# Kernel optimization log

Measured on AMD Instinct MI355X. Metric: run time of the kernel, lower is better.

The kernel has to match this reference:

```python
import jax, jax.numpy as jnp
import numpy as np

N_HEADS = 16


def setup_inputs() -> dict:
    key = jax.random.key(0)
    ks = jax.random.split(key, 9)
    B, S, D = 2, 2048, 1024
    s = 0.02
    return {
        "x": jax.random.normal(ks[0], (B, S, D), dtype=jnp.float32),
        "Wq": jax.random.normal(ks[1], (D, D), dtype=jnp.float32) * s,
        "bq": jax.random.normal(ks[2], (D,), dtype=jnp.float32) * s,
        "Wk": jax.random.normal(ks[3], (D, D), dtype=jnp.float32) * s,
        "bk": jax.random.normal(ks[4], (D,), dtype=jnp.float32) * s,
        "Wv": jax.random.normal(ks[5], (D, D), dtype=jnp.float32) * s,
        "bv": jax.random.normal(ks[6], (D,), dtype=jnp.float32) * s,
        "Wo": jax.random.normal(ks[7], (D, D), dtype=jnp.float32) * s,
        "bo": jax.random.normal(ks[8], (D,), dtype=jnp.float32) * s,
    }


def reference(x, Wq, bq, Wk, bk, Wv, bv, Wo, bo):
    B, S, D = x.shape
    H = N_HEADS
    hd = D // H
    # projections -> [B, H, S, hd]
    def heads(w, b):
        return (x @ w + b).reshape(B, S, H, hd).transpose(0, 2, 1, 3)
    Q, K, V = heads(Wq, bq), heads(Wk, bk), heads(Wv, bv)
    scores = jnp.einsum("bhqd,bhkd->bhqk", Q, K)
    causal = jnp.triu(jnp.ones((S, S), dtype=bool), k=1)  # True above diagonal
    scores = jnp.where(causal, -jnp.inf, scores)
    w = jax.nn.softmax(scores / jnp.sqrt(jnp.float32(hd)), axis=-1)
    ctx = jnp.einsum("bhqk,bhkd->bhqd", w, V).transpose(0, 2, 1, 3).reshape(B, S, D)
    return ctx @ Wo + bo
```

## Files before the change

kernel.cpp:

```cpp
#include <hip/hip_runtime.h>
#include <hip/hip_bf16.h>

typedef __attribute__((ext_vector_type(8))) short short8;
typedef __attribute__((ext_vector_type(4))) float floatx4;
typedef __attribute__((ext_vector_type(4))) int intx4;
typedef __attribute__((ext_vector_type(2))) int intx2;

#define D_MODEL 1024
#define SEQ     2048
#define NB      2
#define NH      16
#define HD      64
#define MROWS   4096
#define CZ      (0.125f * 1.44269504f)

__device__ __forceinline__ floatx4 mfma_bf16(short8 a, short8 b, floatx4 c) {
  return __builtin_amdgcn_mfma_f32_16x16x32_bf16(a, b, c, 0, 0, 0);
}

__device__ __forceinline__ void dma16(const __hip_bfloat16* g, __hip_bfloat16* l) {
  __builtin_amdgcn_global_load_lds(
      (const __attribute__((address_space(1))) void*)g,
      (__attribute__((address_space(3))) void*)l, 16, 0, 0);
}
#define WAIT_VM(n)  __asm__ __volatile__("s_waitcnt vmcnt(" #n ")" ::: "memory")
#define BARRIER()   __asm__ __volatile__("s_barrier" ::: "memory")
#define WAIT_LGKM() __asm__ __volatile__("s_waitcnt lgkmcnt(0)" ::: "memory")

__device__ __forceinline__ int pack2bf(float a, float b) {
  unsigned ua = __builtin_bit_cast(unsigned, a) + 0x8000u;
  unsigned ub = __builtin_bit_cast(unsigned, b) + 0x8000u;
  return (int)__builtin_amdgcn_perm(ub, ua, 0x07060302u);
}

__device__ __forceinline__ int cvtpk(float a, float b) {
  int r;
  __asm__("v_cvt_pk_bf16_f32 %0, %1, %2" : "=v"(r) : "v"(a), "v"(b));
  return r;
}

__global__ void prep_kernel(const float* __restrict__ x, __hip_bfloat16* __restrict__ xb,
                            const float* __restrict__ W0, const float* __restrict__ W1,
                            const float* __restrict__ W2, const float* __restrict__ W3,
                            __hip_bfloat16* __restrict__ T0, __hip_bfloat16* __restrict__ T1,
                            __hip_bfloat16* __restrict__ T2, __hip_bfloat16* __restrict__ T3) {
  const int z = blockIdx.z;
  if (z == 4) {
    const int tid = threadIdx.y * 32 + threadIdx.x;
    const int base = ((blockIdx.y * 32 + blockIdx.x) * 256 + tid) * 16;
#pragma unroll
    for (int c = 0; c < 4; c++) {
      float4 v = *(const float4*)(x + base + c * 4);
      __hip_bfloat16 tmp[4];
      tmp[0] = __float2bfloat16(v.x);
      tmp[1] = __float2bfloat16(v.y);
      tmp[2] = __float2bfloat16(v.z);
      tmp[3] = __float2bfloat16(v.w);
      *(ushort4*)(xb + base + c * 4) = *(ushort4*)tmp;
    }
    return;
  }
  const float* W = (z == 0) ? W0 : (z == 1) ? W1 : (z == 2) ? W2 : W3;
  __hip_bfloat16* Wt = (z == 0) ? T0 : (z == 1) ? T1 : (z == 2) ? T2 : T3;
  __shared__ float tile[32][33];
  int k0 = blockIdx.x * 32, n0 = blockIdx.y * 32;
  int tx = threadIdx.x, ty = threadIdx.y;
#pragma unroll
  for (int i = 0; i < 4; i++)
    tile[ty + 8 * i][tx] = W[(size_t)(k0 + ty + 8 * i) * D_MODEL + n0 + tx];
  __syncthreads();
#pragma unroll
  for (int i = 0; i < 4; i++)
    Wt[(size_t)(n0 + ty + 8 * i) * D_MODEL + k0 + tx] = __float2bfloat16(tile[tx][ty + 8 * i]);
}

template <int MODE>
__global__ __launch_bounds__(256) void gemm_kernel(
    const __hip_bfloat16* __restrict__ X,
    const __hip_bfloat16* __restrict__ Wt0, const __hip_bfloat16* __restrict__ Wt1,
    const __hip_bfloat16* __restrict__ Wt2,
    const float* __restrict__ b0, const float* __restrict__ b1, const float* __restrict__ b2,
    void* __restrict__ out0, void* __restrict__ out1, void* __restrict__ out2) {
  constexpr int MT = (MODE == 0) ? 128 : 64;
  constexpr int I = MT / 32;
  constexpr int NKT = D_MODEL / 32;
  constexpr int SMEM_BYTES = 3 * (MT * 32 + 128 * 32) * 2;

  const int z = blockIdx.y;
  const __hip_bfloat16* Wt = (z == 0) ? Wt0 : (z == 1) ? Wt1 : Wt2;
  const float* bias = (z == 0) ? b0 : (z == 1) ? b1 : b2;
  void* outp = (z == 0) ? out0 : (z == 1) ? out1 : out2;
  const float scale = (MODE == 0 && z == 0) ? CZ : 1.f;

  __shared__ __attribute__((aligned(16))) char smem[SMEM_BYTES];
  __hip_bfloat16* As = (__hip_bfloat16*)smem;
  __hip_bfloat16* Bs = (__hip_bfloat16*)smem + 3 * MT * 32;
  float* Es = (float*)smem;

  const int n0 = blockIdx.x * 128;
  const int m0 = blockIdx.z * MT;
  const int t = threadIdx.x;
  const int lane = t & 63, w = t >> 6;
  const int wm = (w >> 1) * (MT / 2), wn = (w & 1) * 64;
  const int lr = lane & 15;
  const int lq = lane >> 4;

  const __hip_bfloat16* Xp = X + (size_t)m0 * D_MODEL;
  const __hip_bfloat16* Wp = Wt + (size_t)n0 * D_MODEL;

  const int lrow = lane >> 2;
  const int skg = (lane & 3) << 3;
  const int srowA = ((MT == 128) ? (w << 5) : (w << 4)) + lrow;
  const int sbA0 = (((MT == 128) ? (w << 5) : (w << 4)) << 5);
  const int sbA1 = sbA0 + (16 << 5);
  const int srowB = (w << 5) + lrow;
  const int sbB0 = ((w << 5) << 5);
  const int sbB1 = sbB0 + (16 << 5);

#define STAGE_G(kt_, buf_)                                                              \
  {                                                                                     \
    const int kn_ = (kt_) * 32;                                                         \
    __hip_bfloat16* A_ = As + (buf_) * (MT * 32);                                       \
    __hip_bfloat16* B_ = Bs + (buf_) * (128 * 32);                                      \
    dma16(Xp + (size_t)srowA * D_MODEL + kn_ + skg, A_ + sbA0);                         \
    if (MT == 128) dma16(Xp + (size_t)(srowA + 16) * D_MODEL + kn_ + skg, A_ + sbA1);   \
    dma16(Wp + (size_t)srowB * D_MODEL + kn_ + skg, B_ + sbB0);                         \
    dma16(Wp + (size_t)(srowB + 16) * D_MODEL + kn_ + skg, B_ + sbB1);                  \
  }

  floatx4 acc[I][4];
#pragma unroll
  for (int i = 0; i < I; i++)
#pragma unroll
    for (int j = 0; j < 4; j++) acc[i][j] = (floatx4){0.f, 0.f, 0.f, 0.f};

  STAGE_G(0, 0);
  STAGE_G(1, 1);

  int cb = 0;
  for (int kt = 0; kt < NKT; kt++) {
    if (kt < NKT - 1) {
      if constexpr (MODE == 0) WAIT_VM(4);
      else                     WAIT_VM(3);
    } else {
      WAIT_VM(0);
    }
    BARRIER();
    if (kt + 2 < NKT) {
      const int nb = (cb == 0) ? 2 : cb - 1;
      STAGE_G(kt + 2, nb);
    }
    const __hip_bfloat16* Ac = As + cb * (MT * 32);
    const __hip_bfloat16* Bc = Bs + cb * (128 * 32);
    short8 af[I], bfr[4];
#pragma unroll
    for (int i = 0; i < I; i++) af[i] = *(const short8*)&Ac[(wm + i * 16 + lr) * 32 + lq * 8];
#pragma unroll
    for (int j = 0; j < 4; j++) bfr[j] = *(const short8*)&Bc[(wn + j * 16 + lr) * 32 + lq * 8];
#pragma unroll
    for (int i = 0; i < I; i++)
#pragma unroll
      for (int j = 0; j < 4; j++) acc[i][j] = mfma_bf16(af[i], bfr[j], acc[i][j]);
    cb = (cb == 2) ? 0 : cb + 1;
  }
#undef STAGE_G

  float bvj[4];
#pragma unroll
  for (int j = 0; j < 4; j++) bvj[j] = bias[n0 + wn + j * 16 + lr];

  if constexpr (MODE == 1) {
    BARRIER();
#pragma unroll
    for (int i = 0; i < I; i++) {
      const int rowb = wm + i * 16 + lq * 4;
#pragma unroll
      for (int j = 0; j < 4; j++)
#pragma unroll
        for (int r = 0; r < 4; r++)
          Es[(rowb + r) * 132 + wn + j * 16 + lr] = acc[i][j][r] + bvj[j];
    }
    WAIT_LGKM();
    BARRIER();
    const int L = t >> 2, nseg = (t & 3) * 32;
    float* op = (float*)outp + (size_t)(m0 + L) * D_MODEL + n0 + nseg;
    const float* src = &Es[L * 132 + nseg];
#pragma unroll
    for (int k = 0; k < 8; k++) *(float4*)(op + 4 * k) = *(const float4*)(src + 4 * k);
  } else if (z != 2) {
    for (int c = 0; c < 2; c++) {
      BARRIER();
#pragma unroll
      for (int i2 = 0; i2 < 2; i2++) {
        const int i = 2 * c + i2;
        const int rowb = (w >> 1) * 32 + i2 * 16 + lq * 4;
#pragma unroll
        for (int j = 0; j < 4; j++)
#pragma unroll
          for (int r = 0; r < 4; r++)
            Es[(rowb + r) * 132 + wn + j * 16 + lr] = (acc[i][j][r] + bvj[j]) * scale;
      }
      WAIT_LGKM();
      BARRIER();
      const int L = t >> 2, nseg = (t & 3) * 32;
      const int m = m0 + ((L >> 5) << 6) + (c << 5) + (L & 31);
      const int bb = m >> 11, s = m & 2047;
      const int nn = n0 + nseg;
      __hip_bfloat16* op = (__hip_bfloat16*)outp +
          (((size_t)(bb * NH + (nn >> 6)) * SEQ + s) * HD + (nn & 63));
      const float* src = &Es[L * 132 + nseg];
#pragma unroll
      for (int k = 0; k < 4; k++) {
        intx4 pk;
        pk[0] = pack2bf(src[8 * k + 0], src[8 * k + 1]);
        pk[1] = pack2bf(src[8 * k + 2], src[8 * k + 3]);
        pk[2] = pack2bf(src[8 * k + 4], src[8 * k + 5]);
        pk[3] = pack2bf(src[8 * k + 6], src[8 * k + 7]);
        *(intx4*)(op + 8 * k) = pk;
      }
    }
  } else {
    for (int c = 0; c < 2; c++) {
      BARRIER();
#pragma unroll
      for (int j2 = 0; j2 < 2; j2++) {
        const int j = 2 * c + j2;
        const int nl = ((w & 1) << 5) + (j2 << 4) + lr;
#pragma unroll
        for (int i = 0; i < I; i++) {
          const int moff = (w >> 1) * 64 + i * 16 + lq * 4;
          floatx4 v = acc[i][j];
          v[0] += bvj[j]; v[1] += bvj[j]; v[2] += bvj[j]; v[3] += bvj[j];
          *(floatx4*)&Es[nl * 132 + moff] = v;
        }
      }
      WAIT_LGKM();
      BARRIER();
      const int nl = t >> 2, mseg = (t & 3) * 32;
      const int n = n0 + ((nl >> 5) << 6) + (c << 5) + (nl & 31);
      const int s0 = m0 & 2047, bb = m0 >> 11;
      __hip_bfloat16* op = (__hip_bfloat16*)outp +
          (((size_t)(bb * NH + (n >> 6)) * HD + (n & 63)) * SEQ + s0 + mseg);
      const float* src = &Es[nl * 132 + mseg];
#pragma unroll
      for (int k = 0; k < 4; k++) {
        intx4 pk;
        pk[0] = pack2bf(src[8 * k + 0], src[8 * k + 1]);
        pk[1] = pack2bf(src[8 * k + 2], src[8 * k + 3]);
        pk[2] = pack2bf(src[8 * k + 4], src[8 * k + 5]);
        pk[3] = pack2bf(src[8 * k + 6], src[8 * k + 7]);
        *(intx4*)(op + 8 * k) = pk;
      }
    }
  }
}

__global__ __launch_bounds__(256, 4) void attn_kernel(
    const __hip_bfloat16* __restrict__ Q, const __hip_bfloat16* __restrict__ Kg,
    const __hip_bfloat16* __restrict__ Vt, __hip_bfloat16* __restrict__ ctx) {
  const int bh = blockIdx.x;
  const int b = bh >> 4, h = bh & 15;
  const int qt = 31 - blockIdx.y;
  const int t = threadIdx.x, lane = t & 63, w = t >> 6;
  const int lr = lane & 15, lq = lane >> 4;
  const int wr = w & 1, wb = w >> 1;

  __shared__ __attribute__((aligned(16))) __hip_bfloat16 Ks[2][64 * 64];
  __shared__ __attribute__((aligned(16))) __hip_bfloat16 VTs[2][64 * 64];

  const __hip_bfloat16* Qb = Q + (size_t)bh * SEQ * HD;
  const __hip_bfloat16* Kb = Kg + (size_t)bh * SEQ * HD;
  const __hip_bfloat16* Vb = Vt + (size_t)bh * HD * SEQ;

  const int qrow0 = qt * 64 + wr * 32;

  short8 qf[2][2];
#pragma unroll
  for (int rt = 0; rt < 2; rt++)
#pragma unroll
    for (int ks = 0; ks < 2; ks++)
      qf[rt][ks] = *(const short8*)(Qb + (size_t)(qrow0 + rt * 16 + lr) * HD + ks * 32 + lq * 8);

  const int srow = (w << 4) + (lane >> 3);
  const int sgl = lane & 7;
  const int sb0 = (w << 4) << 6;
  const int sb1 = ((w << 4) + 8) << 6;

#define STAGE(tb, nb)                                                                  \
  {                                                                                    \
    const int r0 = srow, r1 = srow + 8;                                                \
    dma16(Kb + ((size_t)((tb) + r0) << 6) + ((sgl ^ (r0 & 7)) << 3), &Ks[nb][sb0]);    \
    dma16(Kb + ((size_t)((tb) + r1) << 6) + ((sgl ^ (r1 & 7)) << 3), &Ks[nb][sb1]);    \
    dma16(Vb + (size_t)r0 * SEQ + (tb) + ((sgl ^ (r0 & 7)) << 3), &VTs[nb][sb0]);      \
    dma16(Vb + (size_t)r1 * SEQ + (tb) + ((sgl ^ (r1 & 7)) << 3), &VTs[nb][sb1]);      \
  }

  const int nkt = qt + 1;
  STAGE(0, 0);

  floatx4 o[2][4];
#pragma unroll
  for (int rt = 0; rt < 2; rt++)
#pragma unroll
    for (int dt = 0; dt < 4; dt++) o[rt][dt] = (floatx4){0.f, 0.f, 0.f, 0.f};
  floatx4 lsacc[2];
  lsacc[0] = (floatx4){0.f, 0.f, 0.f, 0.f};
  lsacc[1] = (floatx4){0.f, 0.f, 0.f, 0.f};

  short8 ones;
#pragma unroll
  for (int j = 0; j < 8; j++) ones[j] = (short)0x3F80;

  const int kfb0 = ((wb << 4) + lr) << 6;
  const int kg0 = ((lq ^ (lr & 7)) << 3);
  const int kg1 = (((4 + lq) ^ (lr & 7)) << 3);
  const int vga = (((wb * 2 + (lq >> 1)) ^ (lr & 7)) << 3) + ((lq & 1) << 2);
  const int vgb = (((4 + wb * 2 + (lq >> 1)) ^ (lr & 7)) << 3) + ((lq & 1) << 2);

  for (int kt = 0; kt < nkt; kt++) {
    WAIT_VM(0);
    BARRIER();
    if (kt + 1 < nkt) STAGE((kt + 1) << 6, (kt + 1) & 1);

    const int kw0 = (kt << 6) + (wb << 4);
    if (kw0 <= qrow0 + 31) {
      const __hip_bfloat16* Kc = Ks[kt & 1];
      const __hip_bfloat16* Vc = VTs[kt & 1];

      short8 kf[2][2];
#pragma unroll
      for (int nt = 0; nt < 2; nt++) {
        kf[0][nt] = *(const short8*)&Kc[(nt << 11) + kfb0 + kg0];
        kf[1][nt] = *(const short8*)&Kc[(nt << 11) + kfb0 + kg1];
      }
      floatx4 s[2][2];
#pragma unroll
      for (int rt = 0; rt < 2; rt++)
#pragma unroll
        for (int nt = 0; nt < 2; nt++) s[rt][nt] = (floatx4){0.f, 0.f, 0.f, 0.f};
#pragma unroll
      for (int ks = 0; ks < 2; ks++)
#pragma unroll
        for (int nt = 0; nt < 2; nt++) {
          s[0][nt] = mfma_bf16(kf[ks][nt], qf[0][ks], s[0][nt]);
          s[1][nt] = mfma_bf16(kf[ks][nt], qf[1][ks], s[1][nt]);
        }

      const bool need_mask = (kw0 + 47 > qrow0);
      short8 pf[2];
#pragma unroll
      for (int rt = 0; rt < 2; rt++) {
        const int q = qrow0 + rt * 16 + lr;
        intx4 pk;
#pragma unroll
        for (int nt = 0; nt < 2; nt++) {
          const int kbase = (kt << 6) + (nt << 5) + (wb << 4) + (lq << 2);
          float x0 = s[rt][nt][0], x1 = s[rt][nt][1], x2 = s[rt][nt][2], x3 = s[rt][nt][3];
          if (need_mask) {
            x0 = (kbase + 0 <= q) ? x0 : -1e30f;
            x1 = (kbase + 1 <= q) ? x1 : -1e30f;
            x2 = (kbase + 2 <= q) ? x2 : -1e30f;
            x3 = (kbase + 3 <= q) ? x3 : -1e30f;
          }
          const float p0 = __builtin_amdgcn_exp2f(x0);
          const float p1 = __builtin_amdgcn_exp2f(x1);
          const float p2 = __builtin_amdgcn_exp2f(x2);
          const float p3 = __builtin_amdgcn_exp2f(x3);
          pk[2 * nt + 0] = cvtpk(p0, p1);
          pk[2 * nt + 1] = cvtpk(p2, p3);
        }
        pf[rt] = __builtin_bit_cast(short8, pk);
      }

      lsacc[0] = mfma_bf16(ones, pf[0], lsacc[0]);
      lsacc[1] = mfma_bf16(ones, pf[1], lsacc[1]);

#pragma unroll
      for (int dt = 0; dt < 4; dt++) {
        const int rb = ((dt << 4) + lr) << 6;
        intx4 vi;
        *(intx2*)&vi = *(const intx2*)&Vc[rb + vga];
        *(((intx2*)&vi) + 1) = *(const intx2*)&Vc[rb + vgb];
        short8 vf = __builtin_bit_cast(short8, vi);
        o[0][dt] = mfma_bf16(vf, pf[0], o[0][dt]);
        o[1][dt] = mfma_bf16(vf, pf[1], o[1][dt]);
      }
    }
  }

  BARRIER();
  if (wb == 1) {
    float* d0 = (float*)&Ks[0][0];
    float* d1 = (float*)&Ks[1][0];
    float* dl = (float*)&VTs[0][0];
    const int base = (wr << 10) + (lane << 4);
#pragma unroll
    for (int dt = 0; dt < 4; dt++) *(floatx4*)&d0[base + (dt << 2)] = o[0][dt];
#pragma unroll
    for (int dt = 0; dt < 4; dt++) *(floatx4*)&d1[base + (dt << 2)] = o[1][dt];
    dl[(wr << 7) + (lane << 1)] = lsacc[0][0];
    dl[(wr << 7) + (lane << 1) + 1] = lsacc[1][0];
    WAIT_LGKM();
  }
  BARRIER();
  if (wb == 0) {
    const float* d0 = (const float*)&Ks[0][0];
    const float* d1 = (const float*)&Ks[1][0];
    const float* dl = (const float*)&VTs[0][0];
    const int base = (wr << 10) + (lane << 4);
#pragma unroll
    for (int dt = 0; dt < 4; dt++) {
      o[0][dt] += *(const floatx4*)&d0[base + (dt << 2)];
      o[1][dt] += *(const floatx4*)&d1[base + (dt << 2)];
    }
    float inv[2];
    inv[0] = 1.f / (lsacc[0][0] + dl[(wr << 7) + (lane << 1)]);
    inv[1] = 1.f / (lsacc[1][0] + dl[(wr << 7) + (lane << 1) + 1]);
#pragma unroll
    for (int rt = 0; rt < 2; rt++) {
      const int row = qrow0 + rt * 16 + lr;
      __hip_bfloat16* cp = ctx + (size_t)b * SEQ * D_MODEL + (size_t)row * D_MODEL + h * HD;
#pragma unroll
      for (int dt = 0; dt < 4; dt++) {
        ushort4 pk;
        __hip_bfloat16* pp = (__hip_bfloat16*)&pk;
#pragma unroll
        for (int r = 0; r < 4; r++) pp[r] = __float2bfloat16(o[rt][dt][r] * inv[rt]);
        *(ushort4*)(cp + (dt << 4) + (lq << 2)) = pk;
      }
    }
  }
#undef STAGE
}

extern "C" void kernel_launch(void* const* d_in, const int* in_sizes, int n_in,
                              void* d_out, int out_size, void* d_ws, size_t ws_size,
                              hipStream_t stream) {
  const float* x  = (const float*)d_in[0];
  const float* Wq = (const float*)d_in[1];
  const float* bq = (const float*)d_in[2];
  const float* Wk = (const float*)d_in[3];
  const float* bk = (const float*)d_in[4];
  const float* Wv = (const float*)d_in[5];
  const float* bv = (const float*)d_in[6];
  const float* Wo = (const float*)d_in[7];
  const float* bo = (const float*)d_in[8];

  char* ws = (char*)d_ws;
  const size_t MB = 1u << 20;
  __hip_bfloat16* xb  = (__hip_bfloat16*)(ws + 0 * MB);
  __hip_bfloat16* wtq = (__hip_bfloat16*)(ws + 8 * MB);
  __hip_bfloat16* wtk = (__hip_bfloat16*)(ws + 10 * MB);
  __hip_bfloat16* wtv = (__hip_bfloat16*)(ws + 12 * MB);
  __hip_bfloat16* wto = (__hip_bfloat16*)(ws + 14 * MB);
  __hip_bfloat16* qb  = (__hip_bfloat16*)(ws + 16 * MB);
  __hip_bfloat16* kb  = (__hip_bfloat16*)(ws + 24 * MB);
  __hip_bfloat16* vt  = (__hip_bfloat16*)(ws + 32 * MB);
  __hip_bfloat16* ctx = xb;

  prep_kernel<<<dim3(32, 32, 5), dim3(32, 8), 0, stream>>>(x, xb, Wq, Wk, Wv, Wo,
                                                           wtq, wtk, wtv, wto);
  gemm_kernel<0><<<dim3(8, 3, 32), 256, 0, stream>>>(xb, wtq, wtk, wtv, bq, bk, bv,
                                                     (void*)qb, (void*)kb, (void*)vt);
  attn_kernel<<<dim3(32, 32), 256, 0, stream>>>(qb, kb, vt, ctx);
  gemm_kernel<1><<<dim3(8, 1, 64), 256, 0, stream>>>(ctx, wto, wto, wto, bo, bo, bo,
                                                     d_out, d_out, d_out);
}
```

Before: 186.7 us.

## Use double-buffered swizzled LDS staging and raise GEMM occupancy hint

Cuts the GEMM LDS pipeline from three stages to two, sizes shared memory as the larger of staging and epilogue needs, and adds a launch-bounds hint of 4 blocks per CU. It also XOR-swizzles the 16-byte column groups on both the DMA writes and the fragment reads to avoid LDS bank conflicts. The aim is higher occupancy and fewer LDS conflicts. In exchange each iteration now waits for all outstanding loads before computing, so there is less prefetch overlap within a block.

```diff
diff --git a/kernel.cpp b/kernel.cpp
--- a/kernel.cpp
+++ b/kernel.cpp
@@ -75,7 +75,7 @@
 }
 
 template <int MODE>
-__global__ __launch_bounds__(256) void gemm_kernel(
+__global__ __launch_bounds__(256, 4) void gemm_kernel(
     const __hip_bfloat16* __restrict__ X,
     const __hip_bfloat16* __restrict__ Wt0, const __hip_bfloat16* __restrict__ Wt1,
     const __hip_bfloat16* __restrict__ Wt2,
@@ -84,7 +84,9 @@
   constexpr int MT = (MODE == 0) ? 128 : 64;
   constexpr int I = MT / 32;
   constexpr int NKT = D_MODEL / 32;
-  constexpr int SMEM_BYTES = 3 * (MT * 32 + 128 * 32) * 2;
+  constexpr int STAGE_BYTES = 2 * (MT * 32 + 128 * 32) * 2;
+  constexpr int EPI_BYTES = 64 * 132 * 4;
+  constexpr int SMEM_BYTES = (STAGE_BYTES > EPI_BYTES) ? STAGE_BYTES : EPI_BYTES;
 
   const int z = blockIdx.y;
   const __hip_bfloat16* Wt = (z == 0) ? Wt0 : (z == 1) ? Wt1 : Wt2;
@@ -94,7 +96,7 @@
 
   __shared__ __attribute__((aligned(16))) char smem[SMEM_BYTES];
   __hip_bfloat16* As = (__hip_bfloat16*)smem;
-  __hip_bfloat16* Bs = (__hip_bfloat16*)smem + 3 * MT * 32;
+  __hip_bfloat16* Bs = (__hip_bfloat16*)smem + 2 * MT * 32;
   float* Es = (float*)smem;
 
   const int n0 = blockIdx.x * 128;
@@ -109,7 +111,7 @@
   const __hip_bfloat16* Wp = Wt + (size_t)n0 * D_MODEL;
 
   const int lrow = lane >> 2;
-  const int skg = (lane & 3) << 3;
+  const int skg = (((lane & 3) ^ ((lane >> 3) & 3)) << 3);
   const int srowA = ((MT == 128) ? (w << 5) : (w << 4)) + lrow;
   const int sbA0 = (((MT == 128) ? (w << 5) : (w << 4)) << 5);
   const int sbA1 = sbA0 + (16 << 5);
@@ -135,33 +137,24 @@
     for (int j = 0; j < 4; j++) acc[i][j] = (floatx4){0.f, 0.f, 0.f, 0.f};
 
   STAGE_G(0, 0);
-  STAGE_G(1, 1);
-
-  int cb = 0;
+
+  const int rcol = ((lq ^ ((lr >> 1) & 3)) << 3);
+
   for (int kt = 0; kt < NKT; kt++) {
-    if (kt < NKT - 1) {
-      if constexpr (MODE == 0) WAIT_VM(4);
-      else                     WAIT_VM(3);
-    } else {
-      WAIT_VM(0);
-    }
+    WAIT_VM(0);
     BARRIER();
-    if (kt + 2 < NKT) {
-      const int nb = (cb == 0) ? 2 : cb - 1;
-      STAGE_G(kt + 2, nb);
-    }
-    const __hip_bfloat16* Ac = As + cb * (MT * 32);
-    const __hip_bfloat16* Bc = Bs + cb * (128 * 32);
+    if (kt + 1 < NKT) STAGE_G(kt + 1, (kt + 1) & 1);
+    const __hip_bfloat16* Ac = As + (kt & 1) * (MT * 32);
+    const __hip_bfloat16* Bc = Bs + (kt & 1) * (128 * 32);
     short8 af[I], bfr[4];
 #pragma unroll
-    for (int i = 0; i < I; i++) af[i] = *(const short8*)&Ac[(wm + i * 16 + lr) * 32 + lq * 8];
-#pragma unroll
-    for (int j = 0; j < 4; j++) bfr[j] = *(const short8*)&Bc[(wn + j * 16 + lr) * 32 + lq * 8];
+    for (int i = 0; i < I; i++) af[i] = *(const short8*)&Ac[(wm + i * 16 + lr) * 32 + rcol];
+#pragma unroll
+    for (int j = 0; j < 4; j++) bfr[j] = *(const short8*)&Bc[(wn + j * 16 + lr) * 32 + rcol];
 #pragma unroll
     for (int i = 0; i < I; i++)
 #pragma unroll
       for (int j = 0; j < 4; j++) acc[i][j] = mfma_bf16(af[i], bfr[j], acc[i][j]);
-    cb = (cb == 2) ? 0 : cb + 1;
   }
 #undef STAGE_G
 
```

Result: no change. 184.6 us (-1.1%).
